# Kernel tuning notes

Hardware: AMD Instinct MI355X
Metric: run time of the kernel (lower is better)

The kernel has to match this reference:

```python
import jax, jax.numpy as jnp
import numpy as np
from functools import partial

N_NODES = 50000
BN_EPS = 1e-5


def _renumber(src, dst, mask, n_nodes):
    # Faithful to extract_batch_edge_idx: kept edges are relabeled by the rank of
    # their node id among the sorted unique node ids APPEARING in kept edges.
    m = mask.astype(jnp.int32)
    appear = jnp.zeros(n_nodes, jnp.int32)
    appear = appear.at[src].max(m)
    appear = appear.at[dst].max(m)
    new_id = jnp.cumsum(appear) - 1  # rank of each appearing node id
    s = jnp.where(mask, new_id[src], 0)
    d = jnp.where(mask, new_id[dst], 0)
    return s, d


def _gcn_conv(x, W, b, src, dst, ew, n):
    # PyG GCNConv: linear, add self-loops, symmetric normalization, scatter-add.
    xw = x @ W                                   # [n, out]
    deg = jax.ops.segment_sum(ew, dst, num_segments=n) + 1.0  # +1 self loop
    dinv = jax.lax.rsqrt(deg)
    norm = dinv[src] * dinv[dst] * ew            # masked edges -> 0 weight
    agg = jax.ops.segment_sum(norm[:, None] * xw[src], dst, num_segments=n)
    agg = agg + (dinv * dinv)[:, None] * xw      # self-loop contribution
    return agg + b


def setup_inputs() -> dict:
    key = jax.random.key(0)
    ks = jax.random.split(key, 8)
    R, N, E, B = 3, N_NODES, 1000000, 2048
    inp, hid, out = 256, 512, 256
    features = jax.random.normal(ks[0], (R, N, inp), jnp.float32)
    W1 = jax.random.normal(ks[1], (inp, hid), jnp.float32) * (1.0 / np.sqrt(inp))
    b1 = jnp.zeros((hid,), jnp.float32)
    W2 = jax.random.normal(ks[2], (hid, out), jnp.float32) * (1.0 / np.sqrt(hid))
    b2 = jnp.zeros((out,), jnp.float32)
    gamma = jnp.ones((hid,), jnp.float32)
    beta = jnp.zeros((hid,), jnp.float32)
    edge_index = jax.random.randint(ks[3], (R, 2, E), 0, N, jnp.int64)
    # distinct, sorted batch node ids (torch code iterates node values)
    batch_nodes = jnp.sort(jax.random.permutation(ks[4], N)[:B]).astype(jnp.int64)
    return {"features": features, "W1": W1, "b1": b1, "W2": W2, "b2": b2,
            "gamma": gamma, "beta": beta, "edge_index": edge_index,
            "batch_nodes": batch_nodes}


def reference(features, W1, b1, W2, b2, gamma, beta, edge_index, batch_nodes):
    R, N, _ = features.shape
    B = batch_nodes.shape[0]
    in_batch = jnp.zeros(N, bool).at[batch_nodes].set(True)
    outs = []
    for r in range(R):  # small fixed relation count
        src, dst = edge_index[r, 0], edge_index[r, 1]
        mask = in_batch[src] & in_batch[dst]
        ew = mask.astype(features.dtype)
        s, d = _renumber(src, dst, mask, N)
        x = features[r, batch_nodes]             # [B, inp]
        h = _gcn_conv(x, W1, b1, s, d, ew, B)    # [B, hid]
        # BatchNorm1d (training mode: biased batch stats)
        mu = h.mean(axis=0)
        var = h.var(axis=0)
        h = (h - mu) * jax.lax.rsqrt(var + BN_EPS) * gamma + beta
        outs.append(_gcn_conv(h, W2, b2, s, d, ew, B))  # [B, out]
    stacked = jnp.stack(outs, axis=0)            # [R, B, out]
    return stacked.reshape(B, -1)                # row-major reshape, as torch
```

## Files before the change

### kernel.cpp

```cpp
#include <hip/hip_runtime.h>
#include <hip/hip_bf16.h>
#include <stdint.h>
#include <stddef.h>

#define RNUM   3
#define NNODES 50000
#define ENUM   1000000
#define BATCH  2048
#define INP    256
#define HID    512
#define OUTC   256
#define BN_EPS 1e-5f

typedef __bf16 bf16x8 __attribute__((ext_vector_type(8)));
typedef float  f32x4  __attribute__((ext_vector_type(4)));

__device__ inline unsigned short f2bf(float f) {
    union { float f; unsigned u; } c; c.f = f;
    unsigned u = c.u;
    return (unsigned short)((u + 0x7fffu + ((u >> 16) & 1u)) >> 16);
}

__device__ inline uint4 pack8(float4 a, float4 b) {
    uint4 r;
    r.x = (unsigned)f2bf(a.x) | ((unsigned)f2bf(a.y) << 16);
    r.y = (unsigned)f2bf(a.z) | ((unsigned)f2bf(a.w) << 16);
    r.z = (unsigned)f2bf(b.x) | ((unsigned)f2bf(b.y) << 16);
    r.w = (unsigned)f2bf(b.z) | ((unsigned)f2bf(b.w) << 16);
    return r;
}

__global__ __launch_bounds__(256) void k_wt(const float* __restrict__ W1,
                                            const float* __restrict__ W2,
                                            unsigned short* __restrict__ W1T,
                                            unsigned short* __restrict__ W2T) {
    __shared__ float T[32][33];
    int z = blockIdx.z;
    const float* W = z ? W2 : W1;
    unsigned short* WT = z ? W2T : W1T;
    int K = z ? HID : INP;
    int N = z ? OUTC : HID;
    int kt = blockIdx.y, nt = blockIdx.x;
    if (kt * 32 >= K || nt * 32 >= N) return;
    int tx = threadIdx.x & 31, ty = threadIdx.x >> 5;
#pragma unroll
    for (int j = 0; j < 4; ++j)
        T[ty + j * 8][tx] = W[(size_t)(kt * 32 + ty + j * 8) * N + nt * 32 + tx];
    __syncthreads();
#pragma unroll
    for (int j = 0; j < 4; ++j)
        WT[(size_t)(nt * 32 + ty + j * 8) * K + kt * 32 + tx] = f2bf(T[tx][ty + j * 8]);
}

__global__ void k_init(int* __restrict__ inv, int* __restrict__ appear,
                       float* __restrict__ deg, float* __restrict__ musum,
                       float* __restrict__ sqsum, int* __restrict__ kcount) {
    int i = blockIdx.x * blockDim.x + threadIdx.x;
    if (i < NNODES) inv[i] = -1;
    if (i < RNUM * BATCH) { appear[i] = 0; deg[i] = 0.0f; }
    if (i < RNUM * HID)   { musum[i] = 0.0f; sqsum[i] = 0.0f; }
    if (i < RNUM)         kcount[i] = 0;
}

__global__ void k_scatter_inv(const int* __restrict__ bn, int* __restrict__ inv) {
    int i = blockIdx.x * blockDim.x + threadIdx.x;
    if (i < BATCH) inv[bn[i]] = i;
}

__global__ void k_mask(const int* __restrict__ edge_index, const int* __restrict__ inv,
                       int* __restrict__ appear, int2* __restrict__ edges,
                       int* __restrict__ kcount) {
    int z = blockIdx.z;
    const int* src = edge_index + (size_t)z * 2 * ENUM;
    const int* dst = src + ENUM;
    int2* ed = edges + (size_t)z * ENUM;
    int* app = appear + z * BATCH;
    int stride = gridDim.x * blockDim.x;
    for (int e4 = blockIdx.x * blockDim.x + threadIdx.x; e4 < ENUM / 4; e4 += stride) {
        int4 s4 = ((const int4*)src)[e4];
        int4 d4 = ((const int4*)dst)[e4];
        int ss[4] = {s4.x, s4.y, s4.z, s4.w};
        int dd[4] = {d4.x, d4.y, d4.z, d4.w};
#pragma unroll
        for (int i = 0; i < 4; ++i) {
            int ps = inv[ss[i]];
            int pd = inv[dd[i]];
            if (ps >= 0 && pd >= 0) {
                int idx = atomicAdd(kcount + z, 1);
                ed[idx] = make_int2(ps, pd);
                app[ps] = 1;
                app[pd] = 1;
            }
        }
    }
}

__global__ __launch_bounds__(1024) void k_scan2048(const int* __restrict__ appear,
                                                   int* __restrict__ rankArr) {
    __shared__ int buf[2][BATCH];
    int z = blockIdx.x;
    const int* ap = appear + z * BATCH;
    int* rk = rankArr + z * BATCH;
    int t = threadIdx.x;
    buf[0][t] = ap[t];
    buf[0][t + 1024] = ap[t + 1024];
    __syncthreads();
    int cur = 0;
    for (int off = 1; off < BATCH; off <<= 1) {
        int nxt = cur ^ 1;
        int i1 = t, i2 = t + 1024;
        buf[nxt][i1] = buf[cur][i1] + (i1 >= off ? buf[cur][i1 - off] : 0);
        buf[nxt][i2] = buf[cur][i2] + (i2 >= off ? buf[cur][i2 - off] : 0);
        __syncthreads();
        cur = nxt;
    }
    rk[t] = buf[cur][t] - 1;
    rk[t + 1024] = buf[cur][t + 1024] - 1;
}

__global__ void k_deg(int2* __restrict__ edges, const int* __restrict__ rankArr,
                      const int* __restrict__ kcount, float* __restrict__ deg) {
    int z = blockIdx.z;
    int K = kcount[z];
    int2* ed = edges + (size_t)z * ENUM;
    const int* rk = rankArr + z * BATCH;
    float* dg = deg + z * BATCH;
    int stride = gridDim.x * blockDim.x;
    for (int e = blockIdx.x * blockDim.x + threadIdx.x; e < K; e += stride) {
        int2 E = ed[e];
        int s = rk[E.x], d = rk[E.y];
        ed[e] = make_int2(s, d);
        atomicAdd(&dg[d], 1.0f);
    }
}


__global__ __launch_bounds__(256) void k_gemm1(
    const float* __restrict__ features, const int* __restrict__ bn,
    const unsigned short* __restrict__ W1T, const float* __restrict__ b1,
    const float* __restrict__ deg, float* __restrict__ xw, float* __restrict__ hbase) {
    __shared__ __align__(16) unsigned short As[64][40];
    __shared__ __align__(16) unsigned short Bs[64][40];
    int z = blockIdx.z;
    const float* feat = features + (size_t)z * NNODES * INP;
    const float* dgz = deg + z * BATCH;
    float* xwz = xw + (size_t)z * BATCH * HID;
    float* hbz = hbase + (size_t)z * BATCH * HID;
    int m0 = blockIdx.y * 64, n0 = blockIdx.x * 64;
    int t = threadIdx.x;
    int ar = t >> 2, aq = t & 3;
    int grow = bn[m0 + ar];
    const float* aptr = feat + (size_t)grow * INP + aq * 8;
    const unsigned short* bptr = W1T + (size_t)(n0 + ar) * INP + aq * 8;

    int lane = t & 63, wave = t >> 6;
    int wm = (wave & 1) * 32, wn = (wave >> 1) * 32;
    int ml = lane & 15, quad = lane >> 4, q8 = quad * 8;

    f32x4 acc[2][2] = {};
    for (int k0 = 0; k0 < INP; k0 += 32) {
        float4 a0 = *(const float4*)(aptr + k0);
        float4 a1 = *(const float4*)(aptr + k0 + 4);
        uint4 bv = *(const uint4*)(bptr + k0);
        *(uint4*)&As[ar][aq * 8] = pack8(a0, a1);
        *(uint4*)&Bs[ar][aq * 8] = bv;
        __syncthreads();
        bf16x8 af[2], bfr[2];
#pragma unroll
        for (int mi = 0; mi < 2; ++mi) af[mi]  = *(const bf16x8*)&As[wm + mi * 16 + ml][q8];
#pragma unroll
        for (int ni = 0; ni < 2; ++ni) bfr[ni] = *(const bf16x8*)&Bs[wn + ni * 16 + ml][q8];
#pragma unroll
        for (int mi = 0; mi < 2; ++mi)
#pragma unroll
            for (int ni = 0; ni < 2; ++ni)
                acc[mi][ni] = __builtin_amdgcn_mfma_f32_16x16x32_bf16(af[mi], bfr[ni], acc[mi][ni], 0, 0, 0);
        __syncthreads();
    }
#pragma unroll
    for (int mi = 0; mi < 2; ++mi)
#pragma unroll
        for (int r = 0; r < 4; ++r) {
            int row = m0 + wm + mi * 16 + quad * 4 + r;
            float d2 = 1.0f / (dgz[row] + 1.0f);
#pragma unroll
            for (int ni = 0; ni < 2; ++ni) {
                int col = n0 + wn + ni * 16 + ml;
                float c = acc[mi][ni][r];
                xwz[(size_t)row * HID + col] = c;
                hbz[(size_t)row * HID + col] = d2 * c + b1[col];
            }
        }
}

__global__ __launch_bounds__(256) void k_gemm2(
    const float* __restrict__ hbase, const float* __restrict__ rstdg,
    const float* __restrict__ shiftc, const unsigned short* __restrict__ W2T,
    const float* __restrict__ b2, const float* __restrict__ deg,
    float* __restrict__ yw, float* __restrict__ out) {
    __shared__ __align__(16) unsigned short As[64][40];
    __shared__ __align__(16) unsigned short Bs[64][40];
    int z = blockIdx.z;
    const float* hz = hbase + (size_t)z * BATCH * HID;
    const float* gz = rstdg + z * HID;
    const float* sz = shiftc + z * HID;
    const float* dgz = deg + z * BATCH;
    float* ywz = yw + (size_t)z * BATCH * OUTC;
    float* oz = out + (size_t)z * BATCH * OUTC;
    int m0 = blockIdx.y * 64, n0 = blockIdx.x * 64;
    int t = threadIdx.x;
    int ar = t >> 2, aq = t & 3;
    const float* aptr = hz + (size_t)(m0 + ar) * HID + aq * 8;
    const unsigned short* bptr = W2T + (size_t)(n0 + ar) * HID + aq * 8;

    int lane = t & 63, wave = t >> 6;
    int wm = (wave & 1) * 32, wn = (wave >> 1) * 32;
    int ml = lane & 15, quad = lane >> 4, q8 = quad * 8;

    f32x4 acc[2][2] = {};
    for (int k0 = 0; k0 < HID; k0 += 32) {
        float4 h0 = *(const float4*)(aptr + k0);
        float4 h1 = *(const float4*)(aptr + k0 + 4);
        float4 g0 = *(const float4*)(gz + k0 + aq * 8);
        float4 g1 = *(const float4*)(gz + k0 + aq * 8 + 4);
        float4 s0 = *(const float4*)(sz + k0 + aq * 8);
        float4 s1 = *(const float4*)(sz + k0 + aq * 8 + 4);
        float4 a0 = make_float4(h0.x * g0.x + s0.x, h0.y * g0.y + s0.y,
                                h0.z * g0.z + s0.z, h0.w * g0.w + s0.w);
        float4 a1 = make_float4(h1.x * g1.x + s1.x, h1.y * g1.y + s1.y,
                                h1.z * g1.z + s1.z, h1.w * g1.w + s1.w);
        uint4 bv = *(const uint4*)(bptr + k0);
        *(uint4*)&As[ar][aq * 8] = pack8(a0, a1);
        *(uint4*)&Bs[ar][aq * 8] = bv;
        __syncthreads();
        bf16x8 af[2], bfr[2];
#pragma unroll
        for (int mi = 0; mi < 2; ++mi) af[mi]  = *(const bf16x8*)&As[wm + mi * 16 + ml][q8];
#pragma unroll
        for (int ni = 0; ni < 2; ++ni) bfr[ni] = *(const bf16x8*)&Bs[wn + ni * 16 + ml][q8];
#pragma unroll
        for (int mi = 0; mi < 2; ++mi)
#pragma unroll
            for (int ni = 0; ni < 2; ++ni)
                acc[mi][ni] = __builtin_amdgcn_mfma_f32_16x16x32_bf16(af[mi], bfr[ni], acc[mi][ni], 0, 0, 0);
        __syncthreads();
    }
#pragma unroll
    for (int mi = 0; mi < 2; ++mi)
#pragma unroll
        for (int r = 0; r < 4; ++r) {
            int row = m0 + wm + mi * 16 + quad * 4 + r;
            float d2 = 1.0f / (dgz[row] + 1.0f);
#pragma unroll
            for (int ni = 0; ni < 2; ++ni) {
                int col = n0 + wn + ni * 16 + ml;
                float c = acc[mi][ni][r];
                ywz[(size_t)row * OUTC + col] = c;
                oz[(size_t)row * OUTC + col] = d2 * c + b2[col];
            }
        }
}

__global__ void k_agg(const int2* __restrict__ edges, const int* __restrict__ kcount,
                      const float* __restrict__ deg, const float* __restrict__ src_mat,
                      float* __restrict__ dst_mat, int ncol) {
    int z = blockIdx.z;
    int K = kcount[z];
    const int2* ed = edges + (size_t)z * ENUM;
    const float* dgz = deg + z * BATCH;
    const float* sm = src_mat + (size_t)z * BATCH * ncol;
    float* dm = dst_mat + (size_t)z * BATCH * ncol;
    for (int e = blockIdx.x; e < K; e += gridDim.x) {
        int2 E = ed[e];
        float w = rsqrtf(dgz[E.x] + 1.0f) * rsqrtf(dgz[E.y] + 1.0f);
        const float* srow = sm + (size_t)E.x * ncol;
        float* drow = dm + (size_t)E.y * ncol;
        for (int c = threadIdx.x; c < ncol; c += blockDim.x)
            atomicAdd(&drow[c], w * srow[c]);
    }
}

__global__ __launch_bounds__(256) void k_bnstats(const float* __restrict__ hbase,
                                                 float* __restrict__ musum,
                                                 float* __restrict__ sqsum) {
    int z = blockIdx.z;
    const float* h = hbase + (size_t)z * BATCH * HID;
    int c0 = threadIdx.x;
    int r0 = blockIdx.x * 32;
    float s1a = 0, s2a = 0, s1b = 0, s2b = 0;
    for (int rr = 0; rr < 32; ++rr) {
        const float* row = h + (size_t)(r0 + rr) * HID;
        float va = row[c0];
        float vb = row[c0 + 256];
        s1a += va; s2a += va * va;
        s1b += vb; s2b += vb * vb;
    }
    atomicAdd(&musum[z * HID + c0], s1a);       atomicAdd(&sqsum[z * HID + c0], s2a);
    atomicAdd(&musum[z * HID + c0 + 256], s1b); atomicAdd(&sqsum[z * HID + c0 + 256], s2b);
}

__global__ void k_bnfinal(const float* __restrict__ musum, const float* __restrict__ sqsum,
                          const float* __restrict__ gamma, const float* __restrict__ beta,
                          float* __restrict__ rstdg, float* __restrict__ shiftc) {
    int z = blockIdx.x;
    int c = threadIdx.x;
    float mu = musum[z * HID + c] * (1.0f / BATCH);
    float ex2 = sqsum[z * HID + c] * (1.0f / BATCH);
    float var = ex2 - mu * mu;
    float g = rsqrtf(var + BN_EPS) * gamma[c];
    rstdg[z * HID + c] = g;
    shiftc[z * HID + c] = beta[c] - mu * g;
}

extern "C" void kernel_launch(void* const* d_in, const int* in_sizes, int n_in,
                              void* d_out, int out_size, void* d_ws, size_t ws_size,
                              hipStream_t stream) {
    const float* features    = (const float*)d_in[0];
    const float* W1          = (const float*)d_in[1];
    const float* b1          = (const float*)d_in[2];
    const float* W2          = (const float*)d_in[3];
    const float* b2          = (const float*)d_in[4];
    const float* gamma       = (const float*)d_in[5];
    const float* beta        = (const float*)d_in[6];
    const int*   edge_index  = (const int*)d_in[7];
    const int*   batch_nodes = (const int*)d_in[8];
    float* out = (float*)d_out;

    char* p = (char*)d_ws;
    size_t cur = 0;
    auto alloc = [&](size_t bytes) {
        void* r = p + cur;
        cur = (cur + bytes + 255) & ~(size_t)255;
        return r;
    };
    int*   inv    = (int*)  alloc(NNODES * sizeof(int));
    int*   appear = (int*)  alloc(RNUM * BATCH * sizeof(int));
    int*   rankA  = (int*)  alloc(RNUM * BATCH * sizeof(int));
    int*   kcount = (int*)  alloc(RNUM * sizeof(int));
    float* deg    = (float*)alloc(RNUM * BATCH * sizeof(float));
    float* musum  = (float*)alloc(RNUM * HID * sizeof(float));
    float* sqsum  = (float*)alloc(RNUM * HID * sizeof(float));
    float* rstdg  = (float*)alloc(RNUM * HID * sizeof(float));
    float* shiftc = (float*)alloc(RNUM * HID * sizeof(float));
    unsigned short* W1T = (unsigned short*)alloc((size_t)HID * INP * sizeof(unsigned short));
    unsigned short* W2T = (unsigned short*)alloc((size_t)OUTC * HID * sizeof(unsigned short));
    int2*  edges  = (int2*) alloc((size_t)RNUM * ENUM * sizeof(int2));
    float* xw     = (float*)alloc((size_t)RNUM * BATCH * HID * sizeof(float));
    float* hbase  = (float*)alloc((size_t)RNUM * BATCH * HID * sizeof(float));
    float* yw     = (float*)alloc((size_t)RNUM * BATCH * OUTC * sizeof(float));
    (void)ws_size; (void)in_sizes; (void)n_in; (void)out_size;

    k_wt<<<dim3(16, 16, 2), 256, 0, stream>>>(W1, W2, W1T, W2T);
    k_init<<<(NNODES + 255) / 256, 256, 0, stream>>>(inv, appear, deg, musum, sqsum, kcount);
    k_scatter_inv<<<BATCH / 256, 256, 0, stream>>>(batch_nodes, inv);

    k_mask<<<dim3(512, 1, RNUM), 256, 0, stream>>>(edge_index, inv, appear, edges, kcount);
    k_scan2048<<<RNUM, 1024, 0, stream>>>(appear, rankA);
    k_deg<<<dim3(64, 1, RNUM), 256, 0, stream>>>(edges, rankA, kcount, deg);

    k_gemm1<<<dim3(HID / 64, BATCH / 64, RNUM), 256, 0, stream>>>(
        features, batch_nodes, W1T, b1, deg, xw, hbase);
    k_agg<<<dim3(256, 1, RNUM), 256, 0, stream>>>(edges, kcount, deg, xw, hbase, HID);

    k_bnstats<<<dim3(64, 1, RNUM), 256, 0, stream>>>(hbase, musum, sqsum);
    k_bnfinal<<<RNUM, HID, 0, stream>>>(musum, sqsum, gamma, beta, rstdg, shiftc);

    k_gemm2<<<dim3(OUTC / 64, BATCH / 64, RNUM), 256, 0, stream>>>(
        hbase, rstdg, shiftc, W2T, b2, deg, yw, out);
    k_agg<<<dim3(256, 1, RNUM), 256, 0, stream>>>(edges, kcount, deg, yw, out, OUTC);
}
```

Measured before the change: 329.5 us.

## Fuse small setup kernels: binary-search inverse map, scan+degree, BN finalize into GEMM2

Replaces the init and scatter-inverse kernels with one kernel that builds the inverse map by binary search over the sorted batch ids. Merges the rank scan with edge relabeling and degree counting, which now run in a single block per relation with shared-memory atomics. Moves the BatchNorm finalization into the second GEMM prologue and vectorizes the aggregation source reads as float4. The aim is fewer launches and less global atomic traffic, but the degree pass now uses only one block per relation, which could serialize the edge loop.

```diff
diff --git a/kernel.cpp b/kernel.cpp
--- a/kernel.cpp
+++ b/kernel.cpp
@@ -52,19 +52,19 @@
         WT[(size_t)(nt * 32 + ty + j * 8) * K + kt * 32 + tx] = f2bf(T[tx][ty + j * 8]);
 }
 
-__global__ void k_init(int* __restrict__ inv, int* __restrict__ appear,
-                       float* __restrict__ deg, float* __restrict__ musum,
-                       float* __restrict__ sqsum, int* __restrict__ kcount) {
+__global__ void k_prep(const int* __restrict__ bn, int* __restrict__ inv,
+                       int* __restrict__ appear, float* __restrict__ deg,
+                       float* __restrict__ musum, float* __restrict__ sqsum,
+                       int* __restrict__ kcount) {
     int i = blockIdx.x * blockDim.x + threadIdx.x;
-    if (i < NNODES) inv[i] = -1;
+    if (i < NNODES) {
+        int lo = 0, hi = BATCH;
+        while (lo < hi) { int mid = (lo + hi) >> 1; if (bn[mid] < i) lo = mid + 1; else hi = mid; }
+        inv[i] = (lo < BATCH && bn[lo] == i) ? lo : -1;
+    }
     if (i < RNUM * BATCH) { appear[i] = 0; deg[i] = 0.0f; }
     if (i < RNUM * HID)   { musum[i] = 0.0f; sqsum[i] = 0.0f; }
     if (i < RNUM)         kcount[i] = 0;
-}
-
-__global__ void k_scatter_inv(const int* __restrict__ bn, int* __restrict__ inv) {
-    int i = blockIdx.x * blockDim.x + threadIdx.x;
-    if (i < BATCH) inv[bn[i]] = i;
 }
 
 __global__ void k_mask(const int* __restrict__ edge_index, const int* __restrict__ inv,
@@ -95,15 +95,20 @@
     }
 }
 
-__global__ __launch_bounds__(1024) void k_scan2048(const int* __restrict__ appear,
-                                                   int* __restrict__ rankArr) {
+__global__ __launch_bounds__(1024) void k_scanDeg(const int* __restrict__ appear,
+                                                  int2* __restrict__ edges,
+                                                  const int* __restrict__ kcount,
+                                                  float* __restrict__ deg) {
     __shared__ int buf[2][BATCH];
+    __shared__ float degs[BATCH];
     int z = blockIdx.x;
     const int* ap = appear + z * BATCH;
-    int* rk = rankArr + z * BATCH;
+    int2* ed = edges + (size_t)z * ENUM;
+    float* dg = deg + z * BATCH;
     int t = threadIdx.x;
     buf[0][t] = ap[t];
     buf[0][t + 1024] = ap[t + 1024];
+    degs[t] = 0.0f; degs[t + 1024] = 0.0f;
     __syncthreads();
     int cur = 0;
     for (int off = 1; off < BATCH; off <<= 1) {
@@ -114,26 +119,18 @@
         __syncthreads();
         cur = nxt;
     }
-    rk[t] = buf[cur][t] - 1;
-    rk[t + 1024] = buf[cur][t + 1024] - 1;
-}
-
-__global__ void k_deg(int2* __restrict__ edges, const int* __restrict__ rankArr,
-                      const int* __restrict__ kcount, float* __restrict__ deg) {
-    int z = blockIdx.z;
     int K = kcount[z];
-    int2* ed = edges + (size_t)z * ENUM;
-    const int* rk = rankArr + z * BATCH;
-    float* dg = deg + z * BATCH;
-    int stride = gridDim.x * blockDim.x;
-    for (int e = blockIdx.x * blockDim.x + threadIdx.x; e < K; e += stride) {
+    for (int e = t; e < K; e += 1024) {
         int2 E = ed[e];
-        int s = rk[E.x], d = rk[E.y];
+        int s = buf[cur][E.x] - 1;
+        int d = buf[cur][E.y] - 1;
         ed[e] = make_int2(s, d);
-        atomicAdd(&dg[d], 1.0f);
-    }
-}
-
+        atomicAdd(&degs[d], 1.0f);
+    }
+    __syncthreads();
+    dg[t] = degs[t];
+    dg[t + 1024] = degs[t + 1024];
+}
 
 __global__ __launch_bounds__(256) void k_gemm1(
     const float* __restrict__ features, const int* __restrict__ bn,
@@ -194,21 +191,34 @@
 }
 
 __global__ __launch_bounds__(256) void k_gemm2(
-    const float* __restrict__ hbase, const float* __restrict__ rstdg,
-    const float* __restrict__ shiftc, const unsigned short* __restrict__ W2T,
+    const float* __restrict__ hbase, const float* __restrict__ musum,
+    const float* __restrict__ sqsum, const float* __restrict__ gamma,
+    const float* __restrict__ beta, const unsigned short* __restrict__ W2T,
     const float* __restrict__ b2, const float* __restrict__ deg,
     float* __restrict__ yw, float* __restrict__ out) {
     __shared__ __align__(16) unsigned short As[64][40];
     __shared__ __align__(16) unsigned short Bs[64][40];
+    __shared__ __align__(16) float gs[HID];
+    __shared__ __align__(16) float ss_[HID];
     int z = blockIdx.z;
     const float* hz = hbase + (size_t)z * BATCH * HID;
-    const float* gz = rstdg + z * HID;
-    const float* sz = shiftc + z * HID;
     const float* dgz = deg + z * BATCH;
     float* ywz = yw + (size_t)z * BATCH * OUTC;
     float* oz = out + (size_t)z * BATCH * OUTC;
     int m0 = blockIdx.y * 64, n0 = blockIdx.x * 64;
     int t = threadIdx.x;
+
+#pragma unroll
+    for (int c = t; c < HID; c += 256) {
+        float mu = musum[z * HID + c] * (1.0f / BATCH);
+        float ex2 = sqsum[z * HID + c] * (1.0f / BATCH);
+        float var = ex2 - mu * mu;
+        float g = rsqrtf(var + BN_EPS) * gamma[c];
+        gs[c] = g;
+        ss_[c] = beta[c] - mu * g;
+    }
+    __syncthreads();
+
     int ar = t >> 2, aq = t & 3;
     const float* aptr = hz + (size_t)(m0 + ar) * HID + aq * 8;
     const unsigned short* bptr = W2T + (size_t)(n0 + ar) * HID + aq * 8;
@@ -221,10 +231,10 @@
     for (int k0 = 0; k0 < HID; k0 += 32) {
         float4 h0 = *(const float4*)(aptr + k0);
         float4 h1 = *(const float4*)(aptr + k0 + 4);
-        float4 g0 = *(const float4*)(gz + k0 + aq * 8);
-        float4 g1 = *(const float4*)(gz + k0 + aq * 8 + 4);
-        float4 s0 = *(const float4*)(sz + k0 + aq * 8);
-        float4 s1 = *(const float4*)(sz + k0 + aq * 8 + 4);
+        float4 g0 = *(const float4*)(gs + k0 + aq * 8);
+        float4 g1 = *(const float4*)(gs + k0 + aq * 8 + 4);
+        float4 s0 = *(const float4*)(ss_ + k0 + aq * 8);
+        float4 s1 = *(const float4*)(ss_ + k0 + aq * 8 + 4);
         float4 a0 = make_float4(h0.x * g0.x + s0.x, h0.y * g0.y + s0.y,
                                 h0.z * g0.z + s0.z, h0.w * g0.w + s0.w);
         float4 a1 = make_float4(h1.x * g1.x + s1.x, h1.y * g1.y + s1.y,
@@ -270,13 +280,19 @@
     const float* dgz = deg + z * BATCH;
     const float* sm = src_mat + (size_t)z * BATCH * ncol;
     float* dm = dst_mat + (size_t)z * BATCH * ncol;
+    int nq = ncol >> 2;
     for (int e = blockIdx.x; e < K; e += gridDim.x) {
         int2 E = ed[e];
         float w = rsqrtf(dgz[E.x] + 1.0f) * rsqrtf(dgz[E.y] + 1.0f);
-        const float* srow = sm + (size_t)E.x * ncol;
+        const float4* srow = (const float4*)(sm + (size_t)E.x * ncol);
         float* drow = dm + (size_t)E.y * ncol;
-        for (int c = threadIdx.x; c < ncol; c += blockDim.x)
-            atomicAdd(&drow[c], w * srow[c]);
+        for (int q = threadIdx.x; q < nq; q += blockDim.x) {
+            float4 v = srow[q];
+            atomicAdd(&drow[q * 4 + 0], w * v.x);
+            atomicAdd(&drow[q * 4 + 1], w * v.y);
+            atomicAdd(&drow[q * 4 + 2], w * v.z);
+            atomicAdd(&drow[q * 4 + 3], w * v.w);
+        }
     }
 }
 
@@ -297,19 +313,6 @@
     }
     atomicAdd(&musum[z * HID + c0], s1a);       atomicAdd(&sqsum[z * HID + c0], s2a);
     atomicAdd(&musum[z * HID + c0 + 256], s1b); atomicAdd(&sqsum[z * HID + c0 + 256], s2b);
-}
-
-__global__ void k_bnfinal(const float* __restrict__ musum, const float* __restrict__ sqsum,
-                          const float* __restrict__ gamma, const float* __restrict__ beta,
-                          float* __restrict__ rstdg, float* __restrict__ shiftc) {
-    int z = blockIdx.x;
-    int c = threadIdx.x;
-    float mu = musum[z * HID + c] * (1.0f / BATCH);
-    float ex2 = sqsum[z * HID + c] * (1.0f / BATCH);
-    float var = ex2 - mu * mu;
-    float g = rsqrtf(var + BN_EPS) * gamma[c];
-    rstdg[z * HID + c] = g;
-    shiftc[z * HID + c] = beta[c] - mu * g;
 }
 
 extern "C" void kernel_launch(void* const* d_in, const int* in_sizes, int n_in,
@@ -335,13 +338,10 @@
     };
     int*   inv    = (int*)  alloc(NNODES * sizeof(int));
     int*   appear = (int*)  alloc(RNUM * BATCH * sizeof(int));
-    int*   rankA  = (int*)  alloc(RNUM * BATCH * sizeof(int));
     int*   kcount = (int*)  alloc(RNUM * sizeof(int));
     float* deg    = (float*)alloc(RNUM * BATCH * sizeof(float));
     float* musum  = (float*)alloc(RNUM * HID * sizeof(float));
     float* sqsum  = (float*)alloc(RNUM * HID * sizeof(float));
-    float* rstdg  = (float*)alloc(RNUM * HID * sizeof(float));
-    float* shiftc = (float*)alloc(RNUM * HID * sizeof(float));
     unsigned short* W1T = (unsigned short*)alloc((size_t)HID * INP * sizeof(unsigned short));
     unsigned short* W2T = (unsigned short*)alloc((size_t)OUTC * HID * sizeof(unsigned short));
     int2*  edges  = (int2*) alloc((size_t)RNUM * ENUM * sizeof(int2));
@@ -351,21 +351,18 @@
     (void)ws_size; (void)in_sizes; (void)n_in; (void)out_size;
 
     k_wt<<<dim3(16, 16, 2), 256, 0, stream>>>(W1, W2, W1T, W2T);
-    k_init<<<(NNODES + 255) / 256, 256, 0, stream>>>(inv, appear, deg, musum, sqsum, kcount);
-    k_scatter_inv<<<BATCH / 256, 256, 0, stream>>>(batch_nodes, inv);
-
+    k_prep<<<(NNODES + 255) / 256, 256, 0, stream>>>(batch_nodes, inv, appear, deg,
+                                                     musum, sqsum, kcount);
     k_mask<<<dim3(512, 1, RNUM), 256, 0, stream>>>(edge_index, inv, appear, edges, kcount);
-    k_scan2048<<<RNUM, 1024, 0, stream>>>(appear, rankA);
-    k_deg<<<dim3(64, 1, RNUM), 256, 0, stream>>>(edges, rankA, kcount, deg);
+    k_scanDeg<<<RNUM, 1024, 0, stream>>>(appear, edges, kcount, deg);
 
     k_gemm1<<<dim3(HID / 64, BATCH / 64, RNUM), 256, 0, stream>>>(
         features, batch_nodes, W1T, b1, deg, xw, hbase);
     k_agg<<<dim3(256, 1, RNUM), 256, 0, stream>>>(edges, kcount, deg, xw, hbase, HID);
 
     k_bnstats<<<dim3(64, 1, RNUM), 256, 0, stream>>>(hbase, musum, sqsum);
-    k_bnfinal<<<RNUM, HID, 0, stream>>>(musum, sqsum, gamma, beta, rstdg, shiftc);
 
     k_gemm2<<<dim3(OUTC / 64, BATCH / 64, RNUM), 256, 0, stream>>>(
-        hbase, rstdg, shiftc, W2T, b2, deg, yw, out);
+        hbase, musum, sqsum, gamma, beta, W2T, b2, deg, yw, out);
     k_agg<<<dim3(256, 1, RNUM), 256, 0, stream>>>(edges, kcount, deg, yw, out, OUTC);
 }
```

After: 365.6 us. 1.11x slower.
